# Optimization experiments

Measured on AMD Instinct MI355X. Metric: run time of the kernel, lower is better.

The kernel has to match this reference:

```python
import jax, jax.numpy as jnp
import numpy as np

BN_EPS = 1e-5

def gated_bottleneck(x2d, cw, cb, g, bta, mean, var, ew, eb):
    # grouped 1x1 conv: each of c1/4 groups mixes 4 adjacent channels
    N = x2d.shape[0]
    y = jnp.einsum('ngj,gj->ng', x2d.reshape(N, -1, 4), cw) + cb
    y = (y - mean) * jax.lax.rsqrt(var + BN_EPS) * g + bta  # BatchNorm1d (eval)
    y = jax.nn.gelu(y, approximate=False)
    return y @ ew.T + eb

def setup_inputs() -> dict:
    key = jax.random.key(0)
    ks = jax.random.split(key, 20)
    c1, c2, bn = 1024, 1024, 256
    d = {
        'x': jax.random.normal(ks[0], (8, 4096, c1), jnp.float32),
        'weight': jax.random.normal(ks[1], (c1, c2), jnp.float32) * (2.0 / c1) ** 0.5,
        'bias': jnp.zeros((c2,), jnp.float32),
        'cw_o': jax.random.normal(ks[2], (bn, 4), jnp.float32),
        'cb_o': jax.random.normal(ks[3], (bn,), jnp.float32),
        'bng_o': jax.random.uniform(ks[4], (bn,), jnp.float32),
        'bnb_o': jax.random.normal(ks[5], (bn,), jnp.float32),
        'bnm_o': jax.random.normal(ks[6], (bn,), jnp.float32),
        'bnv_o': jax.random.uniform(ks[7], (bn,), jnp.float32) + 0.1,
        'ew_o': jax.random.normal(ks[8], (c2, bn), jnp.float32) * 0.05,
        'eb_o': jax.random.normal(ks[9], (c2,), jnp.float32),
        'cw_i': jax.random.normal(ks[10], (bn, 4), jnp.float32),
        'cb_i': jax.random.normal(ks[11], (bn,), jnp.float32),
        'bng_i': jax.random.uniform(ks[12], (bn,), jnp.float32),
        'bnb_i': jax.random.normal(ks[13], (bn,), jnp.float32),
        'bnm_i': jax.random.normal(ks[14], (bn,), jnp.float32),
        'bnv_i': jax.random.uniform(ks[15], (bn,), jnp.float32) + 0.1,
        'ew_i': jax.random.normal(ks[16], (c1, bn), jnp.float32) * 0.05,
        'eb_i': jax.random.normal(ks[17], (c1,), jnp.float32),
        'k': 128,
        'k_in': 128,
    }
    return d

def reference(x, weight, bias, cw_o, cb_o, bng_o, bnb_o, bnm_o, bnv_o, ew_o, eb_o,
              cw_i, cb_i, bng_i, bnb_i, bnm_i, bnv_i, ew_i, eb_i, k, k_in):
    b, l, c1 = x.shape
    c2 = weight.shape[1]
    flat = x.reshape(b * l, c1)

    scores_o = jax.nn.softmax(
        gated_bottleneck(flat, cw_o, cb_o, bng_o, bnb_o, bnm_o, bnv_o, ew_o, eb_o), -1
    ).reshape(b, l, c2)
    sv_o, si_o = jax.lax.top_k(scores_o, k)          # (b,l,k)

    scores_i = jax.nn.softmax(
        gated_bottleneck(flat, cw_i, cb_i, bng_i, bnb_i, bnm_i, bnv_i, ew_i, eb_i), -1
    ).reshape(b, l, c1)
    sv_i, si_i = jax.lax.top_k(scores_i, k_in)        # (b,l,k_in)

    bi = jnp.arange(b)[:, None, None]
    li = jnp.arange(l)[None, :, None]

    # Branch A: output-sparse. einsum over gathered W columns == gather of x@W.
    y = jnp.einsum('blc,co->blo', x, weight)          # (b,l,c2)
    out_k = jnp.take_along_axis(y, si_o, axis=-1) * sv_o
    out_a = jnp.zeros((b, l, c2), x.dtype).at[bi, li, si_o].add(out_k)

    # Branch B: input-sparse. gathered-row einsum == scatter of gated x, then GEMM
    # (top-k indices are distinct so scatter-add builds the exact sparse vector).
    xg = jnp.take_along_axis(x, si_i, axis=-1) * sv_i
    xs = jnp.zeros((b, l, c1), x.dtype).at[bi, li, si_i].add(xg)
    out_b = jnp.einsum('blc,co->blo', xs, weight)

    return out_a + out_b + bias
```

## Files before the change

kernel.cpp:

```cpp
#include <hip/hip_runtime.h>
#include <hip/hip_bf16.h>

typedef __attribute__((ext_vector_type(8))) short short8;
typedef __attribute__((ext_vector_type(8))) _Float16 half8;
typedef __attribute__((ext_vector_type(4))) float f32x4;

#define NROWS 32768
#define CDIM 1024
#define BNC 256
#define TOPK 128
#define NKT 32

struct alignas(8) U4 { unsigned short x, y, z, w; };

__device__ __forceinline__ unsigned short f2bf(float f){
  union { float f; unsigned u; } v; v.f = f;
  unsigned r = v.u + 0x7FFFu + ((v.u >> 16) & 1u);
  return (unsigned short)(r >> 16);
}
__device__ __forceinline__ float bf2f(unsigned short h){
  union { unsigned u; float f; } v; v.u = ((unsigned)h) << 16;
  return v.f;
}
__device__ __forceinline__ unsigned short f2h(float f){
  _Float16 h = (_Float16)f;
  union { _Float16 h; unsigned short u; } v; v.h = h; return v.u;
}
__device__ __forceinline__ float h2f(unsigned short u){
  union { unsigned short u; _Float16 h; } v; v.u = u; return (float)v.h;
}
__device__ __forceinline__ void gl16(const void* g, void* l){
  __builtin_amdgcn_global_load_lds((const __attribute__((address_space(1))) void*)g,
                                   (__attribute__((address_space(3))) void*)l, 16, 0, 0);
}
__device__ __forceinline__ unsigned ldsaddr(const void* p){
  return (unsigned)(uintptr_t)(const __attribute__((address_space(3))) void*)p;
}
__device__ __forceinline__ short8 dsr128(unsigned addr){
  short8 r;
  asm volatile("ds_read_b128 %0, %1" : "=v"(r) : "v"(addr));
  return r;
}
__device__ __forceinline__ half8 s2h(short8 s){ union { short8 s; half8 h; } u; u.s = s; return u.h; }

__device__ __forceinline__ int swzf(int r){ return (r & 3) ^ ((r >> 2) & 1); }
__device__ __forceinline__ int swz(int o){ return o ^ (swzf(o >> 6) << 4); }

__device__ __forceinline__ void stage_tile(const unsigned short* g0, int gstride,
                                           char* lds, int tid){
  #pragma unroll
  for (int i = 0; i < 2; ++i){
    int o = tid * 16 + i * 4096;
    int lb = swz(o);
    gl16((const char*)g0 + (lb >> 6) * gstride + (lb & 63), lds + o);
  }
}
__device__ __forceinline__ int frag_off(int ridx, int lane){
  return ridx * 64 + (((lane >> 4) ^ swzf(ridx)) << 4);
}

__global__ void k_wt(const float* __restrict__ W, unsigned short* __restrict__ Wt){
  __shared__ float t[32][33];
  int tx = threadIdx.x, ty = threadIdx.y;
  int bx = blockIdx.x * 32, by = blockIdx.y * 32;
  for (int i = ty; i < 32; i += 8)
    t[i][tx] = W[(by + i) * CDIM + bx + tx];
  __syncthreads();
  for (int i = ty; i < 32; i += 8)
    Wt[(bx + i) * CDIM + by + tx] = f2h(t[tx][i]);
}

__global__ void k_ecast(const float* __restrict__ eo, const float* __restrict__ ei,
                        unsigned short* __restrict__ ho, unsigned short* __restrict__ hi){
  int i = blockIdx.x * 256 + threadIdx.x;
  ho[i] = f2h(eo[i]);
  hi[i] = f2h(ei[i]);
}

__global__ __launch_bounds__(256) void k_bottleneck(
    const float* __restrict__ x,
    const float* __restrict__ cwo, const float* __restrict__ cbo,
    const float* __restrict__ go,  const float* __restrict__ bto,
    const float* __restrict__ mo,  const float* __restrict__ vo,
    const float* __restrict__ cwi, const float* __restrict__ cbi,
    const float* __restrict__ gi,  const float* __restrict__ bti,
    const float* __restrict__ mi,  const float* __restrict__ vi,
    unsigned short* __restrict__ x16,
    unsigned short* __restrict__ uo, unsigned short* __restrict__ ui)
{
  const int t = threadIdx.x;
  const int r0 = blockIdx.x * 8;
  float4 cwov = ((const float4*)cwo)[t];
  float4 cwiv = ((const float4*)cwi)[t];
  float sco = go[t] * rsqrtf(vo[t] + 1e-5f);
  float sho = bto[t] - mo[t] * sco;
  float cbov = cbo[t];
  float sci = gi[t] * rsqrtf(vi[t] + 1e-5f);
  float shi = bti[t] - mi[t] * sci;
  float cbiv = cbi[t];
  for (int r = 0; r < 8; ++r){
    int row = r0 + r;
    float4 xv = ((const float4*)x)[row * 256 + t];
    U4 xb; xb.x = f2h(xv.x); xb.y = f2h(xv.y); xb.z = f2h(xv.z); xb.w = f2h(xv.w);
    ((U4*)x16)[row * 256 + t] = xb;
    float h = xv.x*cwov.x + xv.y*cwov.y + xv.z*cwov.z + xv.w*cwov.w + cbov;
    h = h * sco + sho;
    float u = 0.5f * h * (1.0f + erff(h * 0.70710678118654752f));
    uo[row*BNC + t] = f2h(u);
    h = xv.x*cwiv.x + xv.y*cwiv.y + xv.z*cwiv.z + xv.w*cwiv.w + cbiv;
    h = h * sci + shi;
    u = 0.5f * h * (1.0f + erff(h * 0.70710678118654752f));
    ui[row*BNC + t] = f2h(u);
  }
}

__global__ __launch_bounds__(256, 3) void k_expand(
    const unsigned short* __restrict__ u16, const unsigned short* __restrict__ e16,
    const float* __restrict__ eb, unsigned short* __restrict__ Lout)
{
  __shared__ alignas(16) char lds[3 * 16384];
  const int tid = threadIdx.x;
  const int lane = tid & 63, w = tid >> 6;
  const int wr = (w >> 1) * 64, wc = (w & 1) * 64;
  int id = blockIdx.x;
  int xcd = id & 7, slot = id >> 3;
  const int row0 = (xcd * 32 + (slot >> 3)) * 128;
  const int col0 = (slot & 7) * 128;
  f32x4 acc[4][4] = {};
  auto stage = [&](int h, int buf){
    char* b = lds + buf * 16384;
    stage_tile(u16 + row0 * BNC + h * 32, 512, b, tid);
    stage_tile(e16 + col0 * BNC + h * 32, 512, b + 8192, tid);
  };
  stage(0, 0);
  stage(1, 1);
  asm volatile("s_waitcnt vmcnt(4)" ::: "memory");
  __builtin_amdgcn_s_barrier();
  const unsigned lbase = ldsaddr(lds);
  const int NK = BNC / 32;
  for (int h = 0; h < NK; ++h){
    unsigned sl = lbase + (h % 3) * 16384;
    short8 af[4], bfr[4];
    #pragma unroll
    for (int m = 0; m < 4; ++m) af[m]  = dsr128(sl + frag_off(wr + m * 16 + (lane & 15), lane));
    #pragma unroll
    for (int n = 0; n < 4; ++n) bfr[n] = dsr128(sl + 8192 + frag_off(wc + n * 16 + (lane & 15), lane));
    if (h + 2 < NK) stage(h + 2, (h + 2) % 3);
    __builtin_amdgcn_s_barrier();
    asm volatile("s_waitcnt lgkmcnt(0)" ::: "memory");
    __builtin_amdgcn_sched_barrier(0);
    __builtin_amdgcn_s_setprio(1);
    #pragma unroll
    for (int m = 0; m < 4; ++m)
      #pragma unroll
      for (int n = 0; n < 4; ++n)
        acc[m][n] = __builtin_amdgcn_mfma_f32_16x16x32_f16(s2h(af[m]), s2h(bfr[n]), acc[m][n], 0, 0, 0);
    __builtin_amdgcn_s_setprio(0);
    if (h + 2 < NK)      asm volatile("s_waitcnt vmcnt(4)" ::: "memory");
    else if (h + 1 < NK) asm volatile("s_waitcnt vmcnt(0)" ::: "memory");
    __builtin_amdgcn_s_barrier();
  }
  #pragma unroll
  for (int n = 0; n < 4; ++n){
    int col = col0 + wc + n * 16 + (lane & 15);
    float ebv = eb[col];
    #pragma unroll
    for (int m = 0; m < 4; ++m){
      int row = row0 + wr + m * 16 + ((lane >> 4) << 2);
      #pragma unroll
      for (int r = 0; r < 4; ++r)
        Lout[(size_t)(row + r) * CDIM + col] = f2h(acc[m][n][r] + ebv);
    }
  }
}

template<bool WRITE_XS>
__global__ __launch_bounds__(256) void k_select(
    const unsigned short* __restrict__ Lg, const unsigned short* __restrict__ xg,
    unsigned short* __restrict__ obf)
{
  const int lane = threadIdx.x & 63;
  const int wv = threadIdx.x >> 6;
  int id = blockIdx.x;
  int xcd = id & 7, rest = id >> 3;
  int q = rest >> 5, b = rest & 31;
  const int row = (xcd * 32 + q) * 128 + b * 4 + wv;
  const unsigned short* Lr = Lg + (size_t)row * CDIM;
  unsigned short hv[16];
  #pragma unroll
  for (int c = 0; c < 2; ++c){
    short8 t8 = ((const short8*)Lr)[c * 64 + lane];
    #pragma unroll
    for (int j = 0; j < 8; ++j) hv[c*8+j] = (unsigned short)t8[j];
  }
  unsigned kx[16];
  #pragma unroll
  for (int j = 0; j < 16; ++j){
    unsigned u = hv[j];
    kx[j] = u ^ ((u & 0x8000u) ? 0xFFFFu : 0x8000u);
  }
  float v[16];
  #pragma unroll
  for (int j = 0; j < 16; ++j) v[j] = h2f(hv[j]);
  float M = v[0];
  #pragma unroll
  for (int j = 1; j < 16; ++j) M = fmaxf(M, v[j]);
  #pragma unroll
  for (int off = 32; off > 0; off >>= 1) M = fmaxf(M, __shfl_xor(M, off));
  float e[16];
  float S = 0.f;
  #pragma unroll
  for (int j = 0; j < 16; ++j){ e[j] = expf(v[j] - M); S += e[j]; }
  #pragma unroll
  for (int off = 32; off > 0; off >>= 1) S += __shfl_xor(S, off);
  unsigned pref = 0;
  for (int bit = 15; bit >= 0; --bit){
    unsigned cand = pref | (1u << bit);
    int c = 0;
    #pragma unroll
    for (int j = 0; j < 16; ++j)
      c += (int)__popcll(__ballot(kx[j] >= cand));
    if (c >= TOPK) pref = cand;
  }
  float invS = 1.0f / S;
  #pragma unroll
  for (int c = 0; c < 2; ++c){
    unsigned short o8[8];
    if (WRITE_XS){
      short8 xv = ((const short8*)(xg + (size_t)row * CDIM))[c * 64 + lane];
      #pragma unroll
      for (int j = 0; j < 8; ++j){
        int jj = c*8 + j;
        float scf = (kx[jj] >= pref) ? e[jj] * invS : 0.f;
        o8[j] = f2h(h2f((unsigned short)xv[j]) * scf);
      }
    } else {
      #pragma unroll
      for (int j = 0; j < 8; ++j){
        int jj = c*8 + j;
        float sc = (kx[jj] >= pref) ? e[jj] * invS : 0.f;
        o8[j] = f2h(sc);
      }
    }
    short8 st;
    #pragma unroll
    for (int j = 0; j < 8; ++j) st[j] = (short)o8[j];
    ((short8*)(obf + (size_t)row * CDIM))[c * 64 + lane] = st;
  }
}

__global__ __launch_bounds__(256, 2) void k_main(
    const unsigned short* __restrict__ x16, const unsigned short* __restrict__ xs16,
    const unsigned short* __restrict__ wt,  const unsigned short* __restrict__ so16,
    const float* __restrict__ bias, float* __restrict__ out)
{
  __shared__ alignas(16) char lds[3 * 24576];
  const int tid = threadIdx.x;
  const int lane = tid & 63, w = tid >> 6;
  const int wr = (w >> 1) * 64, wc = (w & 1) * 64;
  int id = blockIdx.x;
  int xcd = id & 7, sl = id >> 3;
  const int row0 = (xcd * 32 + (sl >> 3)) * 128;
  const int col0 = (sl & 7) * 128;
  f32x4 acc1[4][4] = {}, acc2[4][4] = {};
  auto stage = [&](int kt, int buf){
    char* b = lds + buf * 24576;
    stage_tile(x16  + row0 * CDIM + kt * 32, 2048, b, tid);
    stage_tile(xs16 + row0 * CDIM + kt * 32, 2048, b + 8192, tid);
    stage_tile(wt   + col0 * CDIM + kt * 32, 2048, b + 16384, tid);
  };
  stage(0, 0);
  stage(1, 1);
  asm volatile("s_waitcnt vmcnt(6)" ::: "memory");
  __builtin_amdgcn_s_barrier();
  const unsigned lbase = ldsaddr(lds);
  for (int kt = 0; kt < NKT; ++kt){
    const unsigned slr = lbase + (kt % 3) * 24576;
    short8 a1f[4], a2f[4], bfr[4];
    #pragma unroll
    for (int m = 0; m < 4; ++m){
      int fo = frag_off(wr + m * 16 + (lane & 15), lane);
      a1f[m] = dsr128(slr + fo);
      a2f[m] = dsr128(slr + 8192 + fo);
    }
    #pragma unroll
    for (int n = 0; n < 4; ++n)
      bfr[n] = dsr128(slr + 16384 + frag_off(wc + n * 16 + (lane & 15), lane));
    if (kt + 2 < NKT) stage(kt + 2, (kt + 2) % 3);
    asm volatile("s_waitcnt lgkmcnt(0)" ::: "memory");
    __builtin_amdgcn_sched_barrier(0);
    __builtin_amdgcn_s_setprio(1);
    #pragma unroll
    for (int m = 0; m < 4; ++m)
      #pragma unroll
      for (int n = 0; n < 4; ++n){
        acc1[m][n] = __builtin_amdgcn_mfma_f32_16x16x32_f16(s2h(a1f[m]), s2h(bfr[n]), acc1[m][n], 0, 0, 0);
        acc2[m][n] = __builtin_amdgcn_mfma_f32_16x16x32_f16(s2h(a2f[m]), s2h(bfr[n]), acc2[m][n], 0, 0, 0);
      }
    __builtin_amdgcn_s_setprio(0);
    if (kt + 2 < NKT)      asm volatile("s_waitcnt vmcnt(6)" ::: "memory");
    else if (kt + 1 < NKT) asm volatile("s_waitcnt vmcnt(0)" ::: "memory");
    __builtin_amdgcn_s_barrier();
  }
  #pragma unroll
  for (int n = 0; n < 4; ++n){
    int col = col0 + wc + n * 16 + (lane & 15);
    float bv = bias[col];
    #pragma unroll
    for (int m = 0; m < 4; ++m){
      int row = row0 + wr + m * 16 + ((lane >> 4) << 2);
      #pragma unroll
      for (int r = 0; r < 4; ++r){
        float so = h2f(so16[(size_t)(row + r) * CDIM + col]);
        out[(size_t)(row + r) * CDIM + col] = acc1[m][n][r] * so + acc2[m][n][r] + bv;
      }
    }
  }
}

extern "C" void kernel_launch(void* const* d_in, const int* in_sizes, int n_in,
                              void* d_out, int out_size, void* d_ws, size_t ws_size,
                              hipStream_t stream)
{
  const float* x    = (const float*)d_in[0];
  const float* W    = (const float*)d_in[1];
  const float* bias = (const float*)d_in[2];
  const float* cwo  = (const float*)d_in[3];
  const float* cbo  = (const float*)d_in[4];
  const float* bngo = (const float*)d_in[5];
  const float* bnbo = (const float*)d_in[6];
  const float* bnmo = (const float*)d_in[7];
  const float* bnvo = (const float*)d_in[8];
  const float* ewo  = (const float*)d_in[9];
  const float* ebo  = (const float*)d_in[10];
  const float* cwi  = (const float*)d_in[11];
  const float* cbi  = (const float*)d_in[12];
  const float* bngi = (const float*)d_in[13];
  const float* bnbi = (const float*)d_in[14];
  const float* bnmi = (const float*)d_in[15];
  const float* bnvi = (const float*)d_in[16];
  const float* ewi  = (const float*)d_in[17];
  const float* ebi  = (const float*)d_in[18];
  float* out = (float*)d_out;
  (void)in_sizes; (void)n_in; (void)out_size; (void)ws_size;

  char* ws = (char*)d_ws;
  size_t off = 0;
  auto alloc = [&](size_t bytes){ void* p = ws + off; off += (bytes + 255) & ~(size_t)255; return p; };
  unsigned short* x16  = (unsigned short*)alloc((size_t)NROWS * CDIM * 2);
  unsigned short* xs16 = (unsigned short*)alloc((size_t)NROWS * CDIM * 2);
  unsigned short* so16 = (unsigned short*)alloc((size_t)NROWS * CDIM * 2);
  unsigned short* Lbuf = (unsigned short*)alloc((size_t)NROWS * CDIM * 2);
  unsigned short* uo   = (unsigned short*)alloc((size_t)NROWS * BNC * 2);
  unsigned short* ui   = (unsigned short*)alloc((size_t)NROWS * BNC * 2);
  unsigned short* wtb  = (unsigned short*)alloc((size_t)CDIM * CDIM * 2);
  unsigned short* e16o = (unsigned short*)alloc((size_t)CDIM * BNC * 2);
  unsigned short* e16i = (unsigned short*)alloc((size_t)CDIM * BNC * 2);

  k_wt<<<dim3(32, 32), dim3(32, 8), 0, stream>>>(W, wtb);
  k_ecast<<<dim3(1024), dim3(256), 0, stream>>>(ewo, ewi, e16o, e16i);
  k_bottleneck<<<dim3(NROWS / 8), dim3(256), 0, stream>>>(
      x, cwo, cbo, bngo, bnbo, bnmo, bnvo,
      cwi, cbi, bngi, bnbi, bnmi, bnvi, x16, uo, ui);
  k_expand<<<dim3(2048), dim3(256), 0, stream>>>(uo, e16o, ebo, Lbuf);
  k_select<false><<<dim3(NROWS / 4), dim3(256), 0, stream>>>(Lbuf, nullptr, so16);
  k_expand<<<dim3(2048), dim3(256), 0, stream>>>(ui, e16i, ebi, Lbuf);
  k_select<true><<<dim3(NROWS / 4), dim3(256), 0, stream>>>(Lbuf, x16, xs16);
  k_main<<<dim3(2048), dim3(256), 0, stream>>>(x16, xs16, wtb, so16, bias, out);
}
```

Measured before the change: 366.8 us.

## Fuse expansion GEMM with softmax/top-k selection in one score kernel

Merges k_expand and k_select into a single k_score kernel. Each 512-thread block computes 32 rows of the 1024-wide logits with MFMA, writes them into swizzled LDS, then runs softmax and the radix top-k straight from LDS. This removes the round trip of the fp16 logit buffer through global memory and drops two launches. In exchange, the B operand (e16) is read directly from global memory per wave with no LDS staging, and each block holds 80 KB of LDS, which limits occupancy.

```diff
diff --git a/kernel.cpp b/kernel.cpp
--- a/kernel.cpp
+++ b/kernel.cpp
@@ -13,15 +13,6 @@
 
 struct alignas(8) U4 { unsigned short x, y, z, w; };
 
-__device__ __forceinline__ unsigned short f2bf(float f){
-  union { float f; unsigned u; } v; v.f = f;
-  unsigned r = v.u + 0x7FFFu + ((v.u >> 16) & 1u);
-  return (unsigned short)(r >> 16);
-}
-__device__ __forceinline__ float bf2f(unsigned short h){
-  union { unsigned u; float f; } v; v.u = ((unsigned)h) << 16;
-  return v.f;
-}
 __device__ __forceinline__ unsigned short f2h(float f){
   _Float16 h = (_Float16)f;
   union { _Float16 h; unsigned short u; } v; v.h = h; return v.u;
@@ -114,138 +105,139 @@
   }
 }
 
-__global__ __launch_bounds__(256, 3) void k_expand(
+template<bool WRITE_XS>
+__global__ __launch_bounds__(512, 4) void k_score(
     const unsigned short* __restrict__ u16, const unsigned short* __restrict__ e16,
-    const float* __restrict__ eb, unsigned short* __restrict__ Lout)
-{
-  __shared__ alignas(16) char lds[3 * 16384];
-  const int tid = threadIdx.x;
-  const int lane = tid & 63, w = tid >> 6;
-  const int wr = (w >> 1) * 64, wc = (w & 1) * 64;
-  int id = blockIdx.x;
-  int xcd = id & 7, slot = id >> 3;
-  const int row0 = (xcd * 32 + (slot >> 3)) * 128;
-  const int col0 = (slot & 7) * 128;
-  f32x4 acc[4][4] = {};
-  auto stage = [&](int h, int buf){
-    char* b = lds + buf * 16384;
-    stage_tile(u16 + row0 * BNC + h * 32, 512, b, tid);
-    stage_tile(e16 + col0 * BNC + h * 32, 512, b + 8192, tid);
-  };
-  stage(0, 0);
-  stage(1, 1);
-  asm volatile("s_waitcnt vmcnt(4)" ::: "memory");
-  __builtin_amdgcn_s_barrier();
-  const unsigned lbase = ldsaddr(lds);
-  const int NK = BNC / 32;
-  for (int h = 0; h < NK; ++h){
-    unsigned sl = lbase + (h % 3) * 16384;
-    short8 af[4], bfr[4];
-    #pragma unroll
-    for (int m = 0; m < 4; ++m) af[m]  = dsr128(sl + frag_off(wr + m * 16 + (lane & 15), lane));
-    #pragma unroll
-    for (int n = 0; n < 4; ++n) bfr[n] = dsr128(sl + 8192 + frag_off(wc + n * 16 + (lane & 15), lane));
-    if (h + 2 < NK) stage(h + 2, (h + 2) % 3);
-    __builtin_amdgcn_s_barrier();
-    asm volatile("s_waitcnt lgkmcnt(0)" ::: "memory");
-    __builtin_amdgcn_sched_barrier(0);
-    __builtin_amdgcn_s_setprio(1);
-    #pragma unroll
-    for (int m = 0; m < 4; ++m)
-      #pragma unroll
-      for (int n = 0; n < 4; ++n)
-        acc[m][n] = __builtin_amdgcn_mfma_f32_16x16x32_f16(s2h(af[m]), s2h(bfr[n]), acc[m][n], 0, 0, 0);
-    __builtin_amdgcn_s_setprio(0);
-    if (h + 2 < NK)      asm volatile("s_waitcnt vmcnt(4)" ::: "memory");
-    else if (h + 1 < NK) asm volatile("s_waitcnt vmcnt(0)" ::: "memory");
-    __builtin_amdgcn_s_barrier();
-  }
-  #pragma unroll
-  for (int n = 0; n < 4; ++n){
-    int col = col0 + wc + n * 16 + (lane & 15);
-    float ebv = eb[col];
-    #pragma unroll
-    for (int m = 0; m < 4; ++m){
-      int row = row0 + wr + m * 16 + ((lane >> 4) << 2);
-      #pragma unroll
-      for (int r = 0; r < 4; ++r)
-        Lout[(size_t)(row + r) * CDIM + col] = f2h(acc[m][n][r] + ebv);
-    }
-  }
-}
-
-template<bool WRITE_XS>
-__global__ __launch_bounds__(256) void k_select(
-    const unsigned short* __restrict__ Lg, const unsigned short* __restrict__ xg,
+    const float* __restrict__ eb, const unsigned short* __restrict__ xg,
     unsigned short* __restrict__ obf)
 {
-  const int lane = threadIdx.x & 63;
-  const int wv = threadIdx.x >> 6;
-  int id = blockIdx.x;
-  int xcd = id & 7, rest = id >> 3;
-  int q = rest >> 5, b = rest & 31;
-  const int row = (xcd * 32 + q) * 128 + b * 4 + wv;
-  const unsigned short* Lr = Lg + (size_t)row * CDIM;
-  unsigned short hv[16];
+  __shared__ alignas(16) char lds[81920];
+  const int tid = threadIdx.x;
+  const int lane = tid & 63, wv = tid >> 6;
+  const int row0 = blockIdx.x * 32;
+  const int wc = wv * 128;
+
   #pragma unroll
-  for (int c = 0; c < 2; ++c){
-    short8 t8 = ((const short8*)Lr)[c * 64 + lane];
-    #pragma unroll
-    for (int j = 0; j < 8; ++j) hv[c*8+j] = (unsigned short)t8[j];
-  }
-  unsigned kx[16];
+  for (int i = 0; i < 2; ++i){
+    int o = tid * 16 + i * 8192;
+    int r = o >> 9, g = (o >> 4) & 31;
+    int gs = g ^ (r & 7);
+    gl16((const char*)u16 + (size_t)(row0 + r) * 512 + gs * 16, lds + o);
+  }
+  asm volatile("s_waitcnt vmcnt(0)" ::: "memory");
+  __syncthreads();
+
+  f32x4 acc[2][8] = {};
+  for (int kt = 0; kt < 8; ++kt){
+    short8 af[2];
+    #pragma unroll
+    for (int m = 0; m < 2; ++m){
+      int r = m * 16 + (lane & 15);
+      int g = (kt * 4 + (lane >> 4)) ^ (r & 7);
+      af[m] = *(const short8*)(lds + r * 512 + g * 16);
+    }
+    #pragma unroll
+    for (int half = 0; half < 2; ++half){
+      short8 bfr[4];
+      #pragma unroll
+      for (int n = 0; n < 4; ++n){
+        int col = wc + (half * 4 + n) * 16 + (lane & 15);
+        bfr[n] = *(const short8*)(e16 + (size_t)col * BNC + kt * 32 + ((lane >> 4) << 3));
+      }
+      #pragma unroll
+      for (int m = 0; m < 2; ++m)
+        #pragma unroll
+        for (int n = 0; n < 4; ++n)
+          acc[m][half * 4 + n] =
+            __builtin_amdgcn_mfma_f32_16x16x32_f16(s2h(af[m]), s2h(bfr[n]), acc[m][half * 4 + n], 0, 0, 0);
+    }
+  }
+
+  char* Llds = lds + 16384;
   #pragma unroll
-  for (int j = 0; j < 16; ++j){
-    unsigned u = hv[j];
-    kx[j] = u ^ ((u & 0x8000u) ? 0xFFFFu : 0x8000u);
-  }
-  float v[16];
-  #pragma unroll
-  for (int j = 0; j < 16; ++j) v[j] = h2f(hv[j]);
-  float M = v[0];
-  #pragma unroll
-  for (int j = 1; j < 16; ++j) M = fmaxf(M, v[j]);
-  #pragma unroll
-  for (int off = 32; off > 0; off >>= 1) M = fmaxf(M, __shfl_xor(M, off));
-  float e[16];
-  float S = 0.f;
-  #pragma unroll
-  for (int j = 0; j < 16; ++j){ e[j] = expf(v[j] - M); S += e[j]; }
-  #pragma unroll
-  for (int off = 32; off > 0; off >>= 1) S += __shfl_xor(S, off);
-  unsigned pref = 0;
-  for (int bit = 15; bit >= 0; --bit){
-    unsigned cand = pref | (1u << bit);
-    int c = 0;
-    #pragma unroll
-    for (int j = 0; j < 16; ++j)
-      c += (int)__popcll(__ballot(kx[j] >= cand));
-    if (c >= TOPK) pref = cand;
-  }
-  float invS = 1.0f / S;
-  #pragma unroll
-  for (int c = 0; c < 2; ++c){
-    unsigned short o8[8];
-    if (WRITE_XS){
-      short8 xv = ((const short8*)(xg + (size_t)row * CDIM))[c * 64 + lane];
-      #pragma unroll
-      for (int j = 0; j < 8; ++j){
-        int jj = c*8 + j;
-        float scf = (kx[jj] >= pref) ? e[jj] * invS : 0.f;
-        o8[j] = f2h(h2f((unsigned short)xv[j]) * scf);
-      }
-    } else {
-      #pragma unroll
-      for (int j = 0; j < 8; ++j){
-        int jj = c*8 + j;
-        float sc = (kx[jj] >= pref) ? e[jj] * invS : 0.f;
-        o8[j] = f2h(sc);
-      }
-    }
-    short8 st;
-    #pragma unroll
-    for (int j = 0; j < 8; ++j) st[j] = (short)o8[j];
-    ((short8*)(obf + (size_t)row * CDIM))[c * 64 + lane] = st;
+  for (int n = 0; n < 8; ++n){
+    int col = wc + n * 16 + (lane & 15);
+    float ebv = eb[col];
+    #pragma unroll
+    for (int m = 0; m < 2; ++m)
+      #pragma unroll
+      for (int j = 0; j < 4; ++j){
+        int r = m * 16 + ((lane >> 4) << 2) + j;
+        int g = (col >> 3) ^ (r & 7);
+        *(unsigned short*)(Llds + r * 2048 + g * 16 + (col & 7) * 2) =
+            f2h(acc[m][n][j] + ebv);
+      }
+  }
+  __syncthreads();
+
+  for (int q = 0; q < 4; ++q){
+    int rr = wv * 4 + q;
+    int row = row0 + rr;
+    const char* Lr = Llds + rr * 2048;
+    int sx = rr & 7;
+    unsigned short hv[16];
+    #pragma unroll
+    for (int c = 0; c < 2; ++c){
+      int gidx = c * 64 + lane;
+      short8 t8 = *(const short8*)(Lr + ((gidx ^ sx) << 4));
+      #pragma unroll
+      for (int j = 0; j < 8; ++j) hv[c*8+j] = (unsigned short)t8[j];
+    }
+    unsigned kx[16];
+    #pragma unroll
+    for (int j = 0; j < 16; ++j){
+      unsigned u = hv[j];
+      kx[j] = u ^ ((u & 0x8000u) ? 0xFFFFu : 0x8000u);
+    }
+    float v[16];
+    #pragma unroll
+    for (int j = 0; j < 16; ++j) v[j] = h2f(hv[j]);
+    float M = v[0];
+    #pragma unroll
+    for (int j = 1; j < 16; ++j) M = fmaxf(M, v[j]);
+    #pragma unroll
+    for (int off = 32; off > 0; off >>= 1) M = fmaxf(M, __shfl_xor(M, off));
+    float e[16];
+    float S = 0.f;
+    #pragma unroll
+    for (int j = 0; j < 16; ++j){ e[j] = expf(v[j] - M); S += e[j]; }
+    #pragma unroll
+    for (int off = 32; off > 0; off >>= 1) S += __shfl_xor(S, off);
+    unsigned pref = 0;
+    for (int bit = 15; bit >= 0; --bit){
+      unsigned cand = pref | (1u << bit);
+      int c = 0;
+      #pragma unroll
+      for (int j = 0; j < 16; ++j)
+        c += (int)__popcll(__ballot(kx[j] >= cand));
+      if (c >= TOPK) pref = cand;
+    }
+    float invS = 1.0f / S;
+    #pragma unroll
+    for (int c = 0; c < 2; ++c){
+      int gidx = c * 64 + lane;
+      unsigned short o8[8];
+      if (WRITE_XS){
+        short8 xv = ((const short8*)(xg + (size_t)row * CDIM))[gidx];
+        #pragma unroll
+        for (int j = 0; j < 8; ++j){
+          int jj = c*8 + j;
+          float scf = (kx[jj] >= pref) ? e[jj] * invS : 0.f;
+          o8[j] = f2h(h2f((unsigned short)xv[j]) * scf);
+        }
+      } else {
+        #pragma unroll
+        for (int j = 0; j < 8; ++j){
+          int jj = c*8 + j;
+          float sc = (kx[jj] >= pref) ? e[jj] * invS : 0.f;
+          o8[j] = f2h(sc);
+        }
+      }
+      short8 st;
+      #pragma unroll
+      for (int j = 0; j < 8; ++j) st[j] = (short)o8[j];
+      ((short8*)(obf + (size_t)row * CDIM))[gidx] = st;
+    }
   }
 }
 
@@ -350,7 +342,6 @@
   unsigned short* x16  = (unsigned short*)alloc((size_t)NROWS * CDIM * 2);
   unsigned short* xs16 = (unsigned short*)alloc((size_t)NROWS * CDIM * 2);
   unsigned short* so16 = (unsigned short*)alloc((size_t)NROWS * CDIM * 2);
-  unsigned short* Lbuf = (unsigned short*)alloc((size_t)NROWS * CDIM * 2);
   unsigned short* uo   = (unsigned short*)alloc((size_t)NROWS * BNC * 2);
   unsigned short* ui   = (unsigned short*)alloc((size_t)NROWS * BNC * 2);
   unsigned short* wtb  = (unsigned short*)alloc((size_t)CDIM * CDIM * 2);
@@ -362,9 +353,7 @@
   k_bottleneck<<<dim3(NROWS / 8), dim3(256), 0, stream>>>(
       x, cwo, cbo, bngo, bnbo, bnmo, bnvo,
       cwi, cbi, bngi, bnbi, bnmi, bnvi, x16, uo, ui);
-  k_expand<<<dim3(2048), dim3(256), 0, stream>>>(uo, e16o, ebo, Lbuf);
-  k_select<false><<<dim3(NROWS / 4), dim3(256), 0, stream>>>(Lbuf, nullptr, so16);
-  k_expand<<<dim3(2048), dim3(256), 0, stream>>>(ui, e16i, ebi, Lbuf);
-  k_select<true><<<dim3(NROWS / 4), dim3(256), 0, stream>>>(Lbuf, x16, xs16);
+  k_score<false><<<dim3(NROWS / 32), dim3(512), 0, stream>>>(uo, e16o, ebo, nullptr, so16);
+  k_score<true><<<dim3(NROWS / 32), dim3(512), 0, stream>>>(ui, e16i, ebi, x16, xs16);
   k_main<<<dim3(2048), dim3(256), 0, stream>>>(x16, xs16, wtb, so16, bias, out);
 }
```

Result: slower. 422.8 us (+15.2%).
